# Optimization experiments

Measured on AMD Instinct MI355X. Metric: run time of the kernel, lower is better.

## Reference

```python
import jax, jax.numpy as jnp
import numpy as np

B, S, H, HEADS, STEP = 128, 256, 128, 8, 1


def setup_inputs() -> dict:
    key = jax.random.key(0)
    ks = jax.random.split(key, 20)
    rn = lambda k, shape: jax.random.normal(k, shape, dtype=jnp.float32) * 0.1
    return {
        "A": jax.random.uniform(ks[0], (B, S, 2 * S), dtype=jnp.float32),
        "hidden": jax.random.normal(ks[1], (B, S, H), dtype=jnp.float32),
        "mask": jnp.ones((B, S), dtype=jnp.int32),
        "w_ih": rn(ks[2], (3 * H, 2 * H)),
        "w_hh": rn(ks[3], (3 * H, H)),
        "b_ih": rn(ks[4], (3 * H,)),
        "b_hh": rn(ks[5], (3 * H,)),
        "b_iah": rn(ks[6], (H,)),
        "b_oah": rn(ks[7], (H,)),
        "W_ein": rn(ks[8], (H, H)), "b_ein": rn(ks[9], (H,)),
        "W_eout": rn(ks[10], (H, H)), "b_eout": rn(ks[11], (H,)),
        "W_q0": rn(ks[12], (H, H)), "b_q0": rn(ks[13], (H,)),
        "W_q1": rn(ks[14], (H, H)), "b_q1": rn(ks[15], (H,)),
        "W_q2": rn(ks[16], (H, H)), "b_q2": rn(ks[17], (H,)),
    }


def _forward(A, hidden, mask, w_ih, w_hh, b_ih, b_hh, b_iah, b_oah,
             W_ein, b_ein, W_eout, b_eout, W_q0, b_q0, W_q1, b_q1, W_q2, b_q2):
    b, s, h = hidden.shape
    dk = h // HEADS
    # ---- GNN: gated graph propagation (GRU cell over adjacency messages) ----
    for _ in range(STEP):
        msg_in = A[:, :, :s] @ (hidden @ W_ein.T + b_ein) + b_iah    # [B,S,H]
        msg_out = A[:, :, s:] @ (hidden @ W_eout.T + b_eout) + b_oah  # [B,S,H]
        inputs = jnp.concatenate([msg_in, msg_out], axis=2)           # [B,S,2H]
        gi = inputs @ w_ih.T + b_ih                                   # [B,S,3H]
        gh = hidden @ w_hh.T + b_hh                                   # [B,S,3H]
        i_r, i_i, i_n = jnp.split(gi, 3, axis=2)
        h_r, h_i, h_n = jnp.split(gh, 3, axis=2)
        resetgate = jax.nn.sigmoid(i_r + h_r)
        inputgate = jax.nn.sigmoid(i_i + h_i)
        newgate = jnp.tanh(i_n + resetgate * h_n)
        hidden = hidden - inputgate * (hidden - newgate)
    # ---- query: hidden state of the last valid item in each session ----
    last_idx = jnp.sum(mask, axis=1) - 1
    ht1 = hidden[jnp.arange(b), last_idx]                             # [B,H]
    # ---- LastAttenion: sigmoid score + double softmax readout ----
    q0 = (ht1 @ W_q0.T + b_q0).reshape(b, HEADS, dk)                  # [B,h,dk]
    q1 = (hidden @ W_q1.T + b_q1).reshape(b, s, HEADS, dk).transpose(0, 2, 1, 3)
    q2 = (hidden @ W_q2.T + b_q2).reshape(b, s, HEADS, dk).transpose(0, 2, 1, 3)
    # q0 is expanded over the query axis, so every score row is identical
    alpha = jax.nn.sigmoid(jnp.einsum('bhd,bhjd->bhj', q0, q1))        # [B,h,S]
    alpha = jnp.broadcast_to(alpha[:, :, None, :], (b, HEADS, s, s))   # [B,h,S,S]
    alpha = jax.nn.softmax(alpha, axis=-1)
    row_keep = (mask > 0)[:, None, :, None]                            # [B,1,S,1]
    alpha = jnp.where(row_keep, alpha, -jnp.inf)
    alpha = jax.nn.softmax(2.0 * alpha, axis=1)                        # over heads
    alpha = jnp.where(row_keep, alpha, 0.0)  # guard fully-masked rows (torch would NaN)
    x = jnp.einsum('bhij,bhjd->bhid', alpha, q2)                       # [B,h,S,dk]
    x = x.transpose(0, 2, 1, 3).reshape(b, s, h)                       # [B,S,H]
    a = jnp.sum(x * mask[:, :, None].astype(x.dtype), axis=1)          # [B,H]
    return a


def reference(A, hidden, mask, w_ih, w_hh, b_ih, b_hh, b_iah, b_oah,
              W_ein, b_ein, W_eout, b_eout, W_q0, b_q0, W_q1, b_q1, W_q2, b_q2):
    return _forward(A, hidden, mask, w_ih, w_hh, b_ih, b_hh, b_iah, b_oah,
                    W_ein, b_ein, W_eout, b_eout, W_q0, b_q0, W_q1, b_q1, W_q2, b_q2)
```

## Files before the change

### kernel.cpp

```cpp
#include <hip/hip_runtime.h>
#include <cstdint>
#include <cstddef>

#define BB   128
#define SS   256
#define HH   128
#define NH   8
#define DKK  16

typedef unsigned short u16;
typedef __attribute__((ext_vector_type(8))) short   sh8;
typedef __attribute__((ext_vector_type(4))) float   f32x4;

__device__ __forceinline__ float sigmoidf_(float x) { return 1.f / (1.f + expf(-x)); }

__device__ __forceinline__ u16 f2bf(float x) {
    union { float f; unsigned int u; } v; v.f = x;
    unsigned int r = (v.u + 0x7fffu + ((v.u >> 16) & 1u)) >> 16;
    return (u16)r;
}
__device__ __forceinline__ float bf2f(u16 u) {
    union { unsigned int u; float f; } v; v.u = ((unsigned int)u) << 16;
    return v.f;
}
__device__ __forceinline__ float bflo(unsigned u) {
    union { unsigned u; float f; } v; v.u = u << 16; return v.f;
}
__device__ __forceinline__ float bfhi(unsigned u) {
    union { unsigned u; float f; } v; v.u = u & 0xffff0000u; return v.f;
}

#define BKk 32
#define PK  40

template<int XMODE, int OMODE>
__global__ __launch_bounds__(256) void gemm_mfma(
    const void* __restrict__ Xa, const void* __restrict__ Xc, int ldx, int ldx1, int ksplit,
    long long sXb, long long sXh,
    const u16* __restrict__ Bw, int ldb, long long sBb, long long sBh,
    const float* __restrict__ bias,
    void* __restrict__ Out, long long ldo, long long sOb, long long sOh,
    int K, const u16* __restrict__ hid)
{
    __shared__ __align__(16) char smem[2 * 128 * PK * 2];
    u16* As = (u16*)smem;
    u16* Bs = (u16*)(smem + 128 * PK * 2);

    const int t  = threadIdx.x;
    const int bm = blockIdx.x * 128;
    const int bn = blockIdx.y * 128;
    const long long zb = blockIdx.z >> 1, zh = blockIdx.z & 1;

    const u16* Bp = Bw + zb * sBb + zh * sBh;

    const int wave = t >> 6, lane = t & 63;
    const int wr = (wave >> 1) * 64, wc = (wave & 1) * 64;
    const int fm = lane & 15, fq = lane >> 4;

    f32x4 acc[4][4] = {};

    const int r0  = t >> 2, kk0 = (t & 3) * 8;
    const int r1  = t >> 3, kk1 = (t & 7) * 4;

    uint4  px0, px1, pb0, pb1;
    float4 pf0, pf1, pf2, pf3;

#define LOADX(K0)                                                                    \
    if (XMODE == 1) {                                                                \
        const float* Xf_ = (const float*)Xa + zb * sXb + zh * sXh;                   \
        const float* xp_ = Xf_ + (long long)(bm + r1) * ldx + (K0) + kk1;            \
        pf0 = *(const float4*)(xp_);                                                 \
        pf1 = *(const float4*)(xp_ + 32LL * ldx);                                    \
        pf2 = *(const float4*)(xp_ + 64LL * ldx);                                    \
        pf3 = *(const float4*)(xp_ + 96LL * ldx);                                    \
    } else if (XMODE == 2 && (K0) >= ksplit) {                                       \
        const u16* xp_ = (const u16*)Xc + (long long)(bm + r0) * ldx1                \
                         + ((K0) - ksplit) + kk0;                                    \
        px0 = *(const uint4*)(xp_);                                                  \
        px1 = *(const uint4*)(xp_ + 64LL * ldx1);                                    \
    } else {                                                                         \
        const u16* xp_ = (const u16*)Xa + (long long)(bm + r0) * ldx + (K0) + kk0;   \
        px0 = *(const uint4*)(xp_);                                                  \
        px1 = *(const uint4*)(xp_ + 64LL * ldx);                                     \
    }

#define LOADB(K0)                                                                    \
    {                                                                                \
        const u16* bp_ = Bp + (long long)(bn + r0) * ldb + (K0) + kk0;               \
        pb0 = *(const uint4*)(bp_);                                                  \
        pb1 = *(const uint4*)(bp_ + 64LL * ldb);                                     \
    }

    LOADX(0)
    LOADB(0)

    for (int k0 = 0; k0 < K; k0 += BKk) {
        if (XMODE == 1) {
            ushort4 w0 = { f2bf(pf0.x), f2bf(pf0.y), f2bf(pf0.z), f2bf(pf0.w) };
            ushort4 w1 = { f2bf(pf1.x), f2bf(pf1.y), f2bf(pf1.z), f2bf(pf1.w) };
            ushort4 w2 = { f2bf(pf2.x), f2bf(pf2.y), f2bf(pf2.z), f2bf(pf2.w) };
            ushort4 w3 = { f2bf(pf3.x), f2bf(pf3.y), f2bf(pf3.z), f2bf(pf3.w) };
            *(ushort4*)&As[(r1     ) * PK + kk1] = w0;
            *(ushort4*)&As[(r1 + 32) * PK + kk1] = w1;
            *(ushort4*)&As[(r1 + 64) * PK + kk1] = w2;
            *(ushort4*)&As[(r1 + 96) * PK + kk1] = w3;
        } else {
            *(uint4*)&As[(r0     ) * PK + kk0] = px0;
            *(uint4*)&As[(r0 + 64) * PK + kk0] = px1;
        }
        *(uint4*)&Bs[(r0     ) * PK + kk0] = pb0;
        *(uint4*)&Bs[(r0 + 64) * PK + kk0] = pb1;
        __syncthreads();

        if (k0 + BKk < K) {
            LOADX(k0 + BKk)
            LOADB(k0 + BKk)
        }

        sh8 af[4], bfr[4];
        #pragma unroll
        for (int i = 0; i < 4; i++) af[i]  = *(const sh8*)&As[(wr + i * 16 + fm) * PK + fq * 8];
        #pragma unroll
        for (int j = 0; j < 4; j++) bfr[j] = *(const sh8*)&Bs[(wc + j * 16 + fm) * PK + fq * 8];
        #pragma unroll
        for (int i = 0; i < 4; i++)
            #pragma unroll
            for (int j = 0; j < 4; j++)
                acc[i][j] = __builtin_amdgcn_mfma_f32_16x16x32_bf16(af[i], bfr[j], acc[i][j], 0, 0, 0);
        __syncthreads();
    }
#undef LOADX
#undef LOADB

    if (OMODE != 3) {
        #pragma unroll
        for (int j = 0; j < 4; j++) {
            const int col = bn + wc + j * 16 + fm;
            const float bj = bias ? bias[col] : 0.f;
            #pragma unroll
            for (int i = 0; i < 4; i++) {
                const int row0 = bm + wr + i * 16 + fq * 4;
                if (OMODE == 1) {
                    u16* O = (u16*)Out + zb * sOb + zh * sOh;
                    #pragma unroll
                    for (int r = 0; r < 4; r++)
                        O[(long long)(row0 + r) * ldo + col] = f2bf(acc[i][j][r] + bj);
                } else {
                    u16* O = (u16*)Out + zb * sOb + zh * sOh;
                    ushort4 w = { f2bf(acc[i][j][0] + bj), f2bf(acc[i][j][1] + bj),
                                  f2bf(acc[i][j][2] + bj), f2bf(acc[i][j][3] + bj) };
                    *(ushort4*)&O[(long long)col * ldo + row0] = w;
                }
            }
        }
    } else {
        float* g4s = (float*)smem;
        const int chbase = bn >> 2;
        const int s_t = t >> 3;
        const int cq  = t & 7;
        u16* O = (u16*)Out;
        const int sbase = (wr ? 16 : 0) + fq * 4;
        #pragma unroll
        for (int i = 0; i < 4; i++) {
            #pragma unroll
            for (int j = 0; j < 4; j++) {
                const int q = wc + j * 16 + fm;
                const float bj = bias[bn + q];
                #pragma unroll
                for (int r = 0; r < 4; r++)
                    g4s[(sbase + r) * 132 + q] = acc[i][j][r] + bj;
            }
            __syncthreads();
            {
                const int grow = bm + i * 16 + (s_t < 16 ? s_t : s_t + 48);
                const ushort4 hv = *(const ushort4*)&hid[(long long)grow * HH + chbase + 4 * cq];
                const float hvv[4] = { bf2f(hv.x), bf2f(hv.y), bf2f(hv.z), bf2f(hv.w) };
                ushort4 w;
                u16* wp = (u16*)&w;
                #pragma unroll
                for (int m = 0; m < 4; m++) {
                    f32x4 gv = *(const f32x4*)&g4s[s_t * 132 + 16 * cq + 4 * m];
                    float rg = sigmoidf_(gv[0]);
                    float ig = sigmoidf_(gv[1]);
                    float ng = tanhf(gv[2] + rg * gv[3]);
                    wp[m] = f2bf(hvv[m] - ig * (hvv[m] - ng));
                }
                *(ushort4*)&O[(long long)grow * ldo + chbase + 4 * cq] = w;
            }
            __syncthreads();
        }
    }
}

__global__ __launch_bounds__(256) void k_prepw(
    const float* __restrict__ hidden, u16* __restrict__ h_bf,
    const float* __restrict__ w_ih, const float* __restrict__ w_hh,
    const float* __restrict__ b_ih, const float* __restrict__ b_hh,
    const float* __restrict__ b_iah, const float* __restrict__ b_oah,
    const float* __restrict__ W_ein, const float* __restrict__ b_ein,
    const float* __restrict__ W_eout, const float* __restrict__ b_eout,
    const float* __restrict__ W_q1, const float* __restrict__ b_q1,
    const float* __restrict__ W_q2, const float* __restrict__ b_q2,
    u16* __restrict__ W2bf, float* __restrict__ bias2,
    u16* __restrict__ Wcat, float* __restrict__ biascat,
    u16* __restrict__ Wq12, float* __restrict__ biasq12)
{
    int idx = blockIdx.x * 256 + threadIdx.x;
    {
        float4 v = ((const float4*)hidden)[idx];
        ushort4 w = { f2bf(v.x), f2bf(v.y), f2bf(v.z), f2bf(v.w) };
        ((ushort4*)h_bf)[idx] = w;
    }
    if (idx < 512 * 384) {
        int np = idx / 384, kk = idx % 384;
        int c = np >> 2, g = np & 3;
        float v;
        if (g < 2)       v = (kk < 256) ? w_ih[(g * 128 + c) * 256 + kk]
                                        : w_hh[(g * 128 + c) * 128 + kk - 256];
        else if (g == 2) v = (kk < 256) ? w_ih[(256 + c) * 256 + kk] : 0.f;
        else             v = (kk < 256) ? 0.f : w_hh[(256 + c) * 128 + kk - 256];
        W2bf[idx] = f2bf(v);
    }
    if (idx < 256 * 128) {
        int n = idx >> 7, k = idx & 127;
        Wcat[idx] = f2bf(n < 128 ? W_ein[n * 128 + k] : W_eout[(n - 128) * 128 + k]);
        Wq12[idx] = f2bf(n < 128 ? W_q1[n * 128 + k]  : W_q2[(n - 128) * 128 + k]);
    }
    if (idx < 512) {
        int np = idx, c = np >> 2, g = np & 3;
        float s;
        if (g < 2)       s = b_ih[g * 128 + c] + b_hh[g * 128 + c];
        else if (g == 2) s = b_ih[256 + c];
        else             s = b_hh[256 + c];
        if (g < 3) {
            int n = (g < 2) ? g * 128 + c : 256 + c;
            for (int k = 0; k < 128; k++)
                s += w_ih[n * 256 + k] * b_iah[k] + w_ih[n * 256 + 128 + k] * b_oah[k];
        }
        bias2[np] = s;
    }
    if (idx < 256) {
        biascat[idx] = idx < 128 ? b_ein[idx] : b_eout[idx - 128];
        biasq12[idx] = idx < 128 ? b_q1[idx]  : b_q2[idx - 128];
    }
}

__global__ __launch_bounds__(1024) void k_tail(
    const u16* __restrict__ hnew_bf, const int* __restrict__ mask,
    const u16* __restrict__ q12, const float* __restrict__ Wq0,
    const float* __restrict__ bq0, float* __restrict__ out)
{
    const int b = blockIdx.x, t = threadIdx.x;
    __shared__ float red[1024];
    __shared__ float hs[HH];
    __shared__ float q0s[HH];
    __shared__ float p_s[NH][SS];
    __shared__ float w_s[NH][SS];
    __shared__ int s_nv;

    if (t < 256) red[t] = (float)mask[b * SS + t];
    __syncthreads();
    for (int off = 128; off > 0; off >>= 1) {
        if (t < off) red[t] += red[t + off];
        __syncthreads();
    }
    if (t == 0) s_nv = (int)red[0];
    __syncthreads();
    const int nv = s_nv;
    const int last = (nv - 1) & (SS - 1);

    if (t < HH) hs[t] = bf2f(hnew_bf[((size_t)b * SS + last) * HH + t]);
    __syncthreads();

    {
        const int n = t & 127, kh = t >> 7;
        const float* w = Wq0 + (size_t)n * HH + kh * 16;
        const float* h = hs + kh * 16;
        float s = 0.f;
        #pragma unroll
        for (int k = 0; k < 16; k++) s += h[k] * w[k];
        red[t] = s;
    }
    __syncthreads();
    if (t < HH) {
        float s = bq0[t];
        #pragma unroll
        for (int kh = 0; kh < 8; kh++) s += red[kh * 128 + t];
        q0s[t] = s;
    }
    __syncthreads();

    {
        const int j = t >> 2, q = t & 3;
        const u16* q1r = q12 + ((size_t)b * SS + j) * 256 + q * 32;
        uint4 va = *(const uint4*)(q1r);
        uint4 vb = *(const uint4*)(q1r + 8);
        uint4 vc = *(const uint4*)(q1r + 16);
        uint4 vd = *(const uint4*)(q1r + 24);
        const float* qa = q0s + q * 32;
        float s0 = qa[0]  * bflo(va.x) + qa[1]  * bfhi(va.x)
                 + qa[2]  * bflo(va.y) + qa[3]  * bfhi(va.y)
                 + qa[4]  * bflo(va.z) + qa[5]  * bfhi(va.z)
                 + qa[6]  * bflo(va.w) + qa[7]  * bfhi(va.w)
                 + qa[8]  * bflo(vb.x) + qa[9]  * bfhi(vb.x)
                 + qa[10] * bflo(vb.y) + qa[11] * bfhi(vb.y)
                 + qa[12] * bflo(vb.z) + qa[13] * bfhi(vb.z)
                 + qa[14] * bflo(vb.w) + qa[15] * bfhi(vb.w);
        float s1 = qa[16] * bflo(vc.x) + qa[17] * bfhi(vc.x)
                 + qa[18] * bflo(vc.y) + qa[19] * bfhi(vc.y)
                 + qa[20] * bflo(vc.z) + qa[21] * bfhi(vc.z)
                 + qa[22] * bflo(vc.w) + qa[23] * bfhi(vc.w)
                 + qa[24] * bflo(vd.x) + qa[25] * bfhi(vd.x)
                 + qa[26] * bflo(vd.y) + qa[27] * bfhi(vd.y)
                 + qa[28] * bflo(vd.z) + qa[29] * bfhi(vd.z)
                 + qa[30] * bflo(vd.w) + qa[31] * bfhi(vd.w);
        p_s[2 * q][j]     = sigmoidf_(s0);
        p_s[2 * q + 1][j] = sigmoidf_(s1);
    }
    __syncthreads();

    if (t < 256) {
        const int h = t >> 5, l = t & 31;
        float v[8], m = -1e30f;
        #pragma unroll
        for (int u = 0; u < 8; u++) { v[u] = p_s[h][l * 8 + u]; m = fmaxf(m, v[u]); }
        #pragma unroll
        for (int msk = 1; msk < 32; msk <<= 1) m = fmaxf(m, __shfl_xor(m, msk, 32));
        float sum = 0.f;
        #pragma unroll
        for (int u = 0; u < 8; u++) { v[u] = expf(v[u] - m); sum += v[u]; }
        #pragma unroll
        for (int msk = 1; msk < 32; msk <<= 1) sum += __shfl_xor(sum, msk, 32);
        const float inv = 1.f / sum;
        #pragma unroll
        for (int u = 0; u < 8; u++) p_s[h][l * 8 + u] = v[u] * inv;
    }
    __syncthreads();

    if (t < 256) {
        float e[NH], den = 0.f;
        #pragma unroll
        for (int h = 0; h < NH; h++) { e[h] = expf(2.f * p_s[h][t]); den += e[h]; }
        const float inv = 1.f / den;
        #pragma unroll
        for (int h = 0; h < NH; h++) w_s[h][t] = e[h] * inv;
    }
    __syncthreads();

    {
        const int col = t & 127, jq = t >> 7;
        const int h = col >> 4;
        const u16* q2b = q12 + (size_t)b * SS * 256 + 128 + col;
        float acc = 0.f;
        #pragma unroll 4
        for (int j = jq * 32; j < jq * 32 + 32; j++)
            acc += w_s[h][j] * bf2f(q2b[(size_t)j * 256]);
        red[t] = acc;
    }
    __syncthreads();
    if (t < HH) {
        float s = 0.f;
        #pragma unroll
        for (int jq = 0; jq < 8; jq++) s += red[jq * 128 + t];
        out[(size_t)b * HH + t] = s * (float)nv;
    }
}

extern "C" void kernel_launch(void* const* d_in, const int* in_sizes, int n_in,
                              void* d_out, int out_size, void* d_ws, size_t ws_size,
                              hipStream_t stream)
{
    const float* A      = (const float*)d_in[0];
    const float* hidden = (const float*)d_in[1];
    const int*   mask   = (const int*)d_in[2];
    const float* w_ih   = (const float*)d_in[3];
    const float* w_hh   = (const float*)d_in[4];
    const float* b_ih   = (const float*)d_in[5];
    const float* b_hh   = (const float*)d_in[6];
    const float* b_iah  = (const float*)d_in[7];
    const float* b_oah  = (const float*)d_in[8];
    const float* W_ein  = (const float*)d_in[9];
    const float* b_ein  = (const float*)d_in[10];
    const float* W_eout = (const float*)d_in[11];
    const float* b_eout = (const float*)d_in[12];
    const float* W_q0   = (const float*)d_in[13];
    const float* b_q0   = (const float*)d_in[14];
    const float* W_q1   = (const float*)d_in[15];
    const float* b_q1   = (const float*)d_in[16];
    const float* W_q2   = (const float*)d_in[17];
    const float* b_q2   = (const float*)d_in[18];
    float* out = (float*)d_out;
    char* ws = (char*)d_ws;

    u16*   Et      = (u16*)(ws + 0);
    u16*   Mbuf    = (u16*)(ws + 16777216);
    u16*   q12bf   = (u16*)(ws + 0);
    u16*   hnew_bf = (u16*)(ws + 33554432);
    u16*   h_bf    = (u16*)(ws + 41943040);
    u16*   W2bf    = (u16*)(ws + 50331648);
    u16*   Wcat    = (u16*)(ws + 50724864);
    u16*   Wq12    = (u16*)(ws + 50790400);
    float* bias2   = (float*)(ws + 50855936);
    float* biascat = (float*)(ws + 50857984);
    float* biasq12 = (float*)(ws + 50859008);

    k_prepw<<<4096, 256, 0, stream>>>(hidden, h_bf,
                                      w_ih, w_hh, b_ih, b_hh, b_iah, b_oah,
                                      W_ein, b_ein, W_eout, b_eout,
                                      W_q1, b_q1, W_q2, b_q2,
                                      W2bf, bias2, Wcat, biascat, Wq12, biasq12);

    gemm_mfma<0, 2><<<dim3(256, 2, 1), 256, 0, stream>>>(
        h_bf, nullptr, HH, 0, 0, 0, 0,
        Wcat, HH, 0, 0, biascat,
        Et, 32768, 0, 0, HH, nullptr);

    gemm_mfma<1, 1><<<dim3(2, 1, 256), 256, 0, stream>>>(
        A, nullptr, 512, 0, 0, 131072LL, 256LL,
        Et, 32768, 256LL, 128LL * 32768LL, nullptr,
        Mbuf, 256, 65536LL, 128LL, SS, nullptr);

    gemm_mfma<2, 3><<<dim3(256, 4, 1), 256, 0, stream>>>(
        Mbuf, h_bf, 256, HH, 256, 0, 0,
        W2bf, 384, 0, 0, bias2,
        hnew_bf, HH, 0, 0, 384, h_bf);

    gemm_mfma<0, 1><<<dim3(256, 2, 1), 256, 0, stream>>>(
        hnew_bf, nullptr, HH, 0, 0, 0, 0,
        Wq12, HH, 0, 0, biasq12,
        q12bf, 256, 0, 0, HH, nullptr);

    k_tail<<<BB, 1024, 0, stream>>>(hnew_bf, mask, q12bf, W_q0, b_q0, out);
}
```

Measured before the change: 217.4 us.

## Stage GEMM epilogue through LDS for coalesced stores; split tail over two column halves

After: 221.5 us. No clear change (+1.9%).

```diff
diff --git a/kernel.cpp b/kernel.cpp
--- a/kernel.cpp
+++ b/kernel.cpp
@@ -32,6 +32,7 @@
 
 #define BKk 32
 #define PK  40
+#define LP  136
 
 template<int XMODE, int OMODE>
 __global__ __launch_bounds__(256) void gemm_mfma(
@@ -133,24 +134,48 @@
 #undef LOADB
 
     if (OMODE != 3) {
-        #pragma unroll
-        for (int j = 0; j < 4; j++) {
-            const int col = bn + wc + j * 16 + fm;
-            const float bj = bias ? bias[col] : 0.f;
+        u16* O  = (u16*)Out + zb * sOb + zh * sOh;
+        u16* Ls = (u16*)smem;
+        #pragma unroll
+        for (int hf = 0; hf < 2; hf++) {
+            if (hf) __syncthreads();
+            if (OMODE == 1) {
+                if (wr == hf * 64) {
+                    #pragma unroll
+                    for (int i = 0; i < 4; i++)
+                        #pragma unroll
+                        for (int j = 0; j < 4; j++) {
+                            const int cl = wc + j * 16 + fm;
+                            const float bj = bias ? bias[bn + cl] : 0.f;
+                            #pragma unroll
+                            for (int r = 0; r < 4; r++)
+                                Ls[(i * 16 + fq * 4 + r) * LP + cl] = f2bf(acc[i][j][r] + bj);
+                        }
+                }
+            } else {
+                if (wc == hf * 64) {
+                    #pragma unroll
+                    for (int i = 0; i < 4; i++)
+                        #pragma unroll
+                        for (int j = 0; j < 4; j++) {
+                            const int cl = j * 16 + fm;
+                            const float bj = bias ? bias[bn + hf * 64 + cl] : 0.f;
+                            ushort4 w = { f2bf(acc[i][j][0] + bj), f2bf(acc[i][j][1] + bj),
+                                          f2bf(acc[i][j][2] + bj), f2bf(acc[i][j][3] + bj) };
+                            *(ushort4*)&Ls[cl * LP + wr + i * 16 + fq * 4] = w;
+                        }
+                }
+            }
+            __syncthreads();
+            const int ro = t >> 2;
             #pragma unroll
-            for (int i = 0; i < 4; i++) {
-                const int row0 = bm + wr + i * 16 + fq * 4;
-                if (OMODE == 1) {
-                    u16* O = (u16*)Out + zb * sOb + zh * sOh;
-                    #pragma unroll
-                    for (int r = 0; r < 4; r++)
-                        O[(long long)(row0 + r) * ldo + col] = f2bf(acc[i][j][r] + bj);
-                } else {
-                    u16* O = (u16*)Out + zb * sOb + zh * sOh;
-                    ushort4 w = { f2bf(acc[i][j][0] + bj), f2bf(acc[i][j][1] + bj),
-                                  f2bf(acc[i][j][2] + bj), f2bf(acc[i][j][3] + bj) };
-                    *(ushort4*)&O[(long long)col * ldo + row0] = w;
-                }
+            for (int rr = 0; rr < 4; rr++) {
+                const int c0 = ((t & 3) + rr * 4) * 8;
+                uint4 w = *(const uint4*)&Ls[ro * LP + c0];
+                if (OMODE == 1)
+                    *(uint4*)&O[(long long)(bm + hf * 64 + ro) * ldo + bn + c0] = w;
+                else
+                    *(uint4*)&O[(long long)(bn + hf * 64 + ro) * ldo + bm + c0] = w;
             }
         }
     } else {
@@ -250,21 +275,23 @@
     const u16* __restrict__ q12, const float* __restrict__ Wq0,
     const float* __restrict__ bq0, float* __restrict__ out)
 {
-    const int b = blockIdx.x, t = threadIdx.x;
+    const int b = blockIdx.x, chb = blockIdx.y, t = threadIdx.x;
     __shared__ float red[1024];
+    __shared__ float red2[1024][2];
     __shared__ float hs[HH];
     __shared__ float q0s[HH];
     __shared__ float p_s[NH][SS];
     __shared__ float w_s[NH][SS];
     __shared__ int s_nv;
 
-    if (t < 256) red[t] = (float)mask[b * SS + t];
-    __syncthreads();
-    for (int off = 128; off > 0; off >>= 1) {
-        if (t < off) red[t] += red[t + off];
-        __syncthreads();
-    }
-    if (t == 0) s_nv = (int)red[0];
+    if (t < 256) {
+        int v = mask[b * SS + t];
+        #pragma unroll
+        for (int m = 1; m < 64; m <<= 1) v += __shfl_xor(v, m, 64);
+        if ((t & 63) == 0) red[t >> 6] = (float)v;
+    }
+    __syncthreads();
+    if (t == 0) s_nv = (int)(red[0] + red[1] + red[2] + red[3]);
     __syncthreads();
     const int nv = s_nv;
     const int last = (nv - 1) & (SS - 1);
@@ -348,21 +375,29 @@
     __syncthreads();
 
     {
-        const int col = t & 127, jq = t >> 7;
-        const int h = col >> 4;
+        const int cp = t & 31, jq = t >> 5;
+        const int col = chb * 64 + cp * 2;
+        const int h0 = col >> 4;
         const u16* q2b = q12 + (size_t)b * SS * 256 + 128 + col;
-        float acc = 0.f;
-        #pragma unroll 4
-        for (int j = jq * 32; j < jq * 32 + 32; j++)
-            acc += w_s[h][j] * bf2f(q2b[(size_t)j * 256]);
-        red[t] = acc;
-    }
-    __syncthreads();
-    if (t < HH) {
+        float a0 = 0.f, a1 = 0.f;
+        #pragma unroll
+        for (int u = 0; u < 8; u++) {
+            const int j = jq * 8 + u;
+            const unsigned v = *(const unsigned*)&q2b[(size_t)j * 256];
+            const float w = w_s[h0][j];
+            a0 += w * bflo(v);
+            a1 += w * bfhi(v);
+        }
+        red2[t][0] = a0;
+        red2[t][1] = a1;
+    }
+    __syncthreads();
+    if (t < 64) {
+        const int cp2 = t >> 1, par = t & 1;
         float s = 0.f;
         #pragma unroll
-        for (int jq = 0; jq < 8; jq++) s += red[jq * 128 + t];
-        out[(size_t)b * HH + t] = s * (float)nv;
+        for (int q = 0; q < 32; q++) s += red2[q * 32 + cp2][par];
+        out[(size_t)b * HH + chb * 64 + cp2 * 2 + par] = s * (float)nv;
     }
 }
 
@@ -430,5 +465,5 @@
         Wq12, HH, 0, 0, biasq12,
         q12bf, 256, 0, 0, HH, nullptr);
 
-    k_tail<<<BB, 1024, 0, stream>>>(hnew_bf, mask, q12bf, W_q0, b_q0, out);
-}
+    k_tail<<<dim3(BB, 2), 1024, 0, stream>>>(hnew_bf, mask, q12bf, W_q0, b_q0, out);
+}
```
